# Optimization experiments

Hardware: AMD Instinct MI355X
Metric: run time of the kernel (lower is better)

The kernel has to match this reference:

```python
import jax, jax.numpy as jnp
import numpy as np

N, D, K = 16384, 256, 4096  # encoded vectors, embedding_dim, codebook_size


def setup_inputs() -> dict:
    key = jax.random.key(0)
    k_ze, k_cb = jax.random.split(key)
    ze = jax.random.normal(k_ze, (N, D), dtype=jnp.float32)
    codebook = jax.random.normal(k_cb, (K, D), dtype=jnp.float32)
    return {"ze": ze, "codebook": codebook}


def reference(ze, codebook):
    # Pairwise squared distances: ||ze||^2 + ||e||^2 - 2 ze e^T  -> [N, K]
    sq_norm = (
        jnp.sum(ze ** 2, axis=-1, keepdims=True)
        + jnp.sum(codebook ** 2, axis=1)
        - 2.0 * jnp.matmul(ze, codebook.T)
    )
    indices = jnp.argmin(sq_norm, axis=-1)            # [N]
    zq = jnp.take(codebook, indices, axis=0)          # [N, D] gather

    # VQ losses (stop-gradient mirrors .detach())
    vq_e_loss = jnp.mean((zq - jax.lax.stop_gradient(ze)) ** 2)
    vq_commit_loss = jnp.mean((jax.lax.stop_gradient(zq) - ze) ** 2)

    # perplexity: probs[i] = count_i / 10 (faithful to original, incl. /10)
    counts = jnp.zeros((K,), dtype=jnp.float32).at[indices].add(1.0)
    probs = counts / 10.0
    perplexity = jnp.exp(-jnp.sum(probs * jnp.log(probs + 1e-10)))

    return indices, zq, vq_e_loss, vq_commit_loss, perplexity
```

## Files before the change

### kernel.cpp

```cpp
#include <hip/hip_runtime.h>
#include <math.h>

#define N_TOT 16384
#define DIM   256
#define KCB   4096

typedef __attribute__((ext_vector_type(8)))  short s8v;
typedef __attribute__((ext_vector_type(16))) float f16v;

#define PK_OFF   32832
#define CBF_OFF  163904
#define WS_NEED  4358208ull
#define ZERO_W   36880

__device__ __forceinline__ void gload16(const void* g, void* l) {
  __builtin_amdgcn_global_load_lds(
      (const __attribute__((address_space(1))) unsigned int*)g,
      (__attribute__((address_space(3))) unsigned int*)l, 16, 0, 0);
}

__global__ __launch_bounds__(256)
void cb_prep_k(const float* __restrict__ cb, float* __restrict__ ws) {
  const int t = threadIdx.x, tile = blockIdx.x;
  for (int i = tile * 256 + t; i < ZERO_W; i += 128 * 256) ws[KCB + i] = 0.0f;

  const int col = t >> 3, j = t & 7;
  const int c0  = tile * 32;
  ushort* tb = (ushort*)((char*)ws + CBF_OFF) + (size_t)tile * 16384;
  const float* src = cb + (size_t)(c0 + col) * DIM;
  float s = 0.0f;
  #pragma unroll
  for (int ks = 0; ks < 16; ++ks) {
    #pragma unroll
    for (int kh = 0; kh < 2; ++kh) {
      float x = src[ks * 16 + kh * 8 + j];
      s += x * x;
      unsigned xb = __float_as_uint(x);
      unsigned hb = xb & 0xFFFF0000u;
      float lf = x - __uint_as_float(hb);
      tb[ks * 512 + kh * 256 + t]        = (ushort)(xb >> 16);
      tb[8192 + ks * 512 + kh * 256 + t] = (ushort)(__float_as_uint(lf) >> 16);
    }
  }
  s += __shfl_down(s, 4, 8);
  s += __shfl_down(s, 2, 8);
  s += __shfl_down(s, 1, 8);
  if (j == 0) ws[c0 + col] = s;
}

#define AP 260

__global__ __launch_bounds__(512, 2)
void vq_mfma_k(const float* __restrict__ ze, float* __restrict__ ws) {
  __shared__ __align__(16) char ldsU[66560];

  const int t    = threadIdx.x;
  const int lane = t & 63;
  const int w    = t >> 6;
  const int ln31 = lane & 31;
  const int hl   = lane >> 5;
  const int mb   = blockIdx.x >> 2;
  const int cq   = blockIdx.x & 3;
  const int m0   = mb * 256;

  const float* cbn = ws;
  unsigned long long* pk = (unsigned long long*)((char*)ws + PK_OFF);
  const char* cbF = (const char*)ws + CBF_OFF;

  s8v ah[16], al[16];
  float* Af = (float*)ldsU;
  for (int c = 0; c < 4; ++c) {
    __syncthreads();
    {
      int r  = t >> 3;
      int f0 = t & 7;
      const float* src = ze + (size_t)(m0 + c * 64 + r) * DIM;
      #pragma unroll
      for (int i = 0; i < 8; ++i) {
        int f = f0 + 8 * i;
        *(float4*)&Af[r * AP + f * 4] = *(const float4*)(src + f * 4);
      }
    }
    __syncthreads();
    if ((w >> 1) == c) {
      int rl = (w & 1) * 32 + ln31;
      #pragma unroll
      for (int ks = 0; ks < 16; ++ks) {
        float4 x0 = *(const float4*)&Af[rl * AP + ks * 16 + hl * 8];
        float4 x1 = *(const float4*)&Af[rl * AP + ks * 16 + hl * 8 + 4];
        float xs[8] = {x0.x, x0.y, x0.z, x0.w, x1.x, x1.y, x1.z, x1.w};
        #pragma unroll
        for (int j = 0; j < 8; ++j) {
          unsigned xb = __float_as_uint(xs[j]);
          unsigned hb = xb & 0xFFFF0000u;
          float lf = xs[j] - __uint_as_float(hb);
          ah[ks][j] = (short)(xb >> 16);
          al[ks][j] = (short)(__float_as_uint(lf) >> 16);
        }
      }
    }
  }
  __syncthreads();

  char* bufs0 = ldsU;
  char* bufs1 = ldsU + 32768;
  const char* qbase = cbF + (size_t)cq * 32 * 32768;

  {
    const char* g = qbase + (size_t)w * 4096 + (size_t)lane * 16;
    char* lp = bufs0 + w * 4096;
    #pragma unroll
    for (int ii = 0; ii < 4; ++ii) gload16(g + ii * 1024, lp + ii * 1024);
  }

  float best[16];
  int   bidx[16];
  #pragma unroll
  for (int r = 0; r < 16; ++r) { best[r] = -1e30f; bidx[r] = 0; }

  #pragma unroll 1
  for (int tt = 0; tt < 32; ++tt) {
    __syncthreads();
    if (tt + 1 < 32) {
      const char* g = qbase + (size_t)(tt + 1) * 32768 + (size_t)w * 4096 + (size_t)lane * 16;
      char* lp = ((tt + 1) & 1 ? bufs1 : bufs0) + w * 4096;
      #pragma unroll
      for (int ii = 0; ii < 4; ++ii) gload16(g + ii * 1024, lp + ii * 1024);
    }

    const int   c0      = cq * 1024 + tt * 32;
    const float half_cv = 0.5f * cbn[c0 + ln31];
    const char* bc      = (tt & 1) ? bufs1 : bufs0;

    f16v hh, xx;
    #pragma unroll
    for (int r = 0; r < 16; ++r) { hh[r] = 0.0f; xx[r] = 0.0f; }

    #pragma unroll
    for (int ks = 0; ks < 16; ++ks) {
      s8v bh = *(const s8v*)(bc + ks * 1024 + lane * 16);
      s8v bl = *(const s8v*)(bc + 16384 + ks * 1024 + lane * 16);
      hh = __builtin_amdgcn_mfma_f32_32x32x16_bf16(ah[ks], bh, hh, 0, 0, 0);
      xx = __builtin_amdgcn_mfma_f32_32x32x16_bf16(ah[ks], bl, xx, 0, 0, 0);
      xx = __builtin_amdgcn_mfma_f32_32x32x16_bf16(al[ks], bh, xx, 0, 0, 0);
    }

    #pragma unroll
    for (int r = 0; r < 16; ++r) {
      float s = hh[r] + xx[r] - half_cv;
      if (s > best[r]) { best[r] = s; bidx[r] = c0 + ln31; }
    }
  }

  #pragma unroll
  for (int r = 0; r < 16; ++r) {
    float s = best[r];
    int   c = bidx[r];
    #pragma unroll
    for (int mk = 1; mk < 32; mk <<= 1) {
      float os = __shfl_xor(s, mk, 64);
      int   oc = __shfl_xor(c, mk, 64);
      if (os > s || (os == s && oc < c)) { s = os; c = oc; }
    }
    if (ln31 == 0) {
      int row = m0 + w * 32 + (r & 3) + 8 * (r >> 2) + 4 * hl;
      unsigned u = __float_as_uint(s);
      unsigned enc = (u & 0x80000000u) ? ~u : (u | 0x80000000u);
      unsigned long long p = ((unsigned long long)enc << 32) | (unsigned)(KCB - 1 - c);
      atomicMax(&pk[row], p);
    }
  }
}

__global__ __launch_bounds__(256)
void gather_k(const float* __restrict__ ze, const float* __restrict__ cb,
              float* __restrict__ ws, float* __restrict__ out) {
  __shared__ int sIdx[64];
  const int t  = threadIdx.x;
  const int m0 = blockIdx.x * 64;
  float* counts   = ws + KCB;
  float* loss_sum = ws + 2 * KCB;
  const unsigned long long* pk = (const unsigned long long*)((const char*)ws + PK_OFF);

  if (t < 64) {
    unsigned long long p = pk[m0 + t];
    int col = KCB - 1 - (int)(unsigned)(p & 0xFFFFFFFFull);
    out[m0 + t] = (float)col;
    sIdx[t] = col;
    atomicAdd(&counts[col], 1.0f);
  }
  __syncthreads();

  float* out_zq = out + N_TOT;
  const int w = t >> 6, ln = t & 63;
  float lsum = 0.0f;
  #pragma unroll
  for (int p = 0; p < 16; ++p) {
    int r = w + 4 * p;
    float4 cvv = *(const float4*)(cb + (size_t)sIdx[r] * DIM + ln * 4);
    float4 zv  = *(const float4*)(ze + (size_t)(m0 + r) * DIM + ln * 4);
    *(float4*)(out_zq + (size_t)(m0 + r) * DIM + ln * 4) = cvv;
    float dx = cvv.x - zv.x, dy = cvv.y - zv.y, dz = cvv.z - zv.z, dw = cvv.w - zv.w;
    lsum += dx * dx + dy * dy + dz * dz + dw * dw;
  }
  #pragma unroll
  for (int off = 32; off > 0; off >>= 1) lsum += __shfl_down(lsum, off, 64);
  if (ln == 0) atomicAdd(loss_sum, lsum);
}

__global__ void zero_ws_k(float* __restrict__ ws, int nw) {
  int i = blockIdx.x * 256 + threadIdx.x;
  if (i < nw) ws[KCB + i] = 0.0f;
}

__global__ void cbnorm_k(const float* __restrict__ cb, float* __restrict__ ws) {
  int row  = blockIdx.x * 4 + (threadIdx.x >> 6);
  int lane = threadIdx.x & 63;
  float4 v = *(const float4*)(cb + (size_t)row * DIM + lane * 4);
  float s = v.x*v.x + v.y*v.y + v.z*v.z + v.w*v.w;
  #pragma unroll
  for (int off = 32; off > 0; off >>= 1) s += __shfl_down(s, off, 64);
  if (lane == 0) ws[row] = s;
}

#define FBM 32
#define FBN 64
#define FBD 128
__global__ __launch_bounds__(256, 4)
void vq_main_k(const float* __restrict__ ze, const float* __restrict__ cb,
               float* __restrict__ ws, float* __restrict__ out) {
  __shared__ float As[FBM * FBD];
  __shared__ float Bs[FBN * FBD];
  __shared__ float red_d[FBM * 16];
  __shared__ int   red_i[FBM * 16];
  __shared__ int   sIdx[FBM];

  const int t  = threadIdx.x;
  const int tx = t & 15;
  const int ty = t >> 4;
  const int m0 = blockIdx.x * FBM;

  const float* cbn = ws;
  float* counts    = ws + KCB;
  float* loss_sum  = ws + 2 * KCB;

  float best0 = 1e30f, best1 = 1e30f;
  int   bidx0 = 0,     bidx1 = 0;
  const int sA = ty & 7;
  const int sB = tx & 7;

  for (int kt = 0; kt < KCB / FBN; ++kt) {
    float cbnj[4];
    #pragma unroll
    for (int j = 0; j < 4; ++j) cbnj[j] = cbn[kt * FBN + tx + 16 * j];
    float acc[2][4];
    #pragma unroll
    for (int i = 0; i < 2; ++i)
      #pragma unroll
      for (int j = 0; j < 4; ++j) acc[i][j] = 0.0f;

    for (int dc = 0; dc < DIM / FBD; ++dc) {
      __syncthreads();
      {
        int c  = t & 31;
        int rb = t >> 5;
        #pragma unroll
        for (int p = 0; p < 4; ++p) {
          int r = rb + 8 * p;
          float4 v = *(const float4*)(ze + (size_t)(m0 + r) * DIM + dc * FBD + c * 4);
          *(float4*)&As[r * FBD + ((c ^ (r & 7)) << 2)] = v;
        }
        #pragma unroll
        for (int p = 0; p < 8; ++p) {
          int r = rb + 8 * p;
          float4 v = *(const float4*)(cb + (size_t)(kt * FBN + r) * DIM + dc * FBD + c * 4);
          *(float4*)&Bs[r * FBD + ((c ^ (r & 7)) << 2)] = v;
        }
      }
      __syncthreads();
      #pragma unroll 8
      for (int ds = 0; ds < FBD / 4; ++ds) {
        float4 a0 = *(const float4*)&As[ty * FBD + ((ds ^ sA) << 2)];
        float4 a1 = *(const float4*)&As[(ty + 16) * FBD + ((ds ^ sA) << 2)];
        float4 b[4];
        #pragma unroll
        for (int j = 0; j < 4; ++j)
          b[j] = *(const float4*)&Bs[(tx + 16 * j) * FBD + ((ds ^ sB) << 2)];
        #pragma unroll
        for (int j = 0; j < 4; ++j) {
          acc[0][j] = fmaf(a0.x, b[j].x, acc[0][j]);
          acc[0][j] = fmaf(a0.y, b[j].y, acc[0][j]);
          acc[0][j] = fmaf(a0.z, b[j].z, acc[0][j]);
          acc[0][j] = fmaf(a0.w, b[j].w, acc[0][j]);
          acc[1][j] = fmaf(a1.x, b[j].x, acc[1][j]);
          acc[1][j] = fmaf(a1.y, b[j].y, acc[1][j]);
          acc[1][j] = fmaf(a1.z, b[j].z, acc[1][j]);
          acc[1][j] = fmaf(a1.w, b[j].w, acc[1][j]);
        }
      }
    }
    #pragma unroll
    for (int j = 0; j < 4; ++j) {
      int kg = kt * FBN + tx + 16 * j;
      float d0 = cbnj[j] - 2.0f * acc[0][j];
      float d1 = cbnj[j] - 2.0f * acc[1][j];
      if (d0 < best0) { best0 = d0; bidx0 = kg; }
      if (d1 < best1) { best1 = d1; bidx1 = kg; }
    }
  }

  __syncthreads();
  red_d[ty * 16 + tx] = best0;        red_i[ty * 16 + tx] = bidx0;
  red_d[(ty + 16) * 16 + tx] = best1; red_i[(ty + 16) * 16 + tx] = bidx1;
  __syncthreads();

  if (t < FBM) {
    float bd = red_d[t * 16]; int bi = red_i[t * 16];
    #pragma unroll
    for (int q = 1; q < 16; ++q) {
      float d = red_d[t * 16 + q]; int i2 = red_i[t * 16 + q];
      if (d < bd || (d == bd && i2 < bi)) { bd = d; bi = i2; }
    }
    out[m0 + t] = (float)bi;
    sIdx[t] = bi;
    atomicAdd(&counts[bi], 1.0f);
  }
  __syncthreads();

  float* out_zq = out + N_TOT;
  const int wv = t >> 6, ln = t & 63;
  float lsum = 0.0f;
  #pragma unroll
  for (int p = 0; p < 8; ++p) {
    int r = wv + 4 * p;
    float4 cvv = *(const float4*)(cb + (size_t)sIdx[r] * DIM + ln * 4);
    float4 zv  = *(const float4*)(ze + (size_t)(m0 + r) * DIM + ln * 4);
    *(float4*)(out_zq + (size_t)(m0 + r) * DIM + ln * 4) = cvv;
    float dx = cvv.x - zv.x, dy = cvv.y - zv.y, dz = cvv.z - zv.z, dw = cvv.w - zv.w;
    lsum += dx*dx + dy*dy + dz*dz + dw*dw;
  }
  #pragma unroll
  for (int off = 32; off > 0; off >>= 1) lsum += __shfl_down(lsum, off, 64);
  if (ln == 0) atomicAdd(loss_sum, lsum);
}

__global__ void finalize_k(const float* __restrict__ ws, float* __restrict__ out) {
  __shared__ float red[256];
  int t = threadIdx.x;
  const float* counts = ws + KCB;
  float s = 0.0f;
  for (int k = t; k < KCB; k += 256) {
    float p = counts[k] * 0.1f;
    s += p * logf(p + 1e-10f);
  }
  red[t] = s;
  __syncthreads();
  for (int q = 128; q > 0; q >>= 1) { if (t < q) red[t] += red[t + q]; __syncthreads(); }
  if (t == 0) {
    float loss = ws[2 * KCB] / (float)((size_t)N_TOT * DIM);
    float* o = out + N_TOT + (size_t)N_TOT * DIM;
    o[0] = loss;
    o[1] = loss;
    o[2] = expf(-red[0]);
  }
}

extern "C" void kernel_launch(void* const* d_in, const int* in_sizes, int n_in,
                              void* d_out, int out_size, void* d_ws, size_t ws_size,
                              hipStream_t stream) {
  const float* ze = (const float*)d_in[0];
  const float* cb = (const float*)d_in[1];
  float* out = (float*)d_out;
  float* ws  = (float*)d_ws;

  if (ws_size >= WS_NEED) {
    cb_prep_k<<<128, 256, 0, stream>>>(cb, ws);
    vq_mfma_k<<<256, 512, 0, stream>>>(ze, ws);
    gather_k<<<N_TOT / 64, 256, 0, stream>>>(ze, cb, ws, out);
  } else {
    zero_ws_k<<<(KCB + 1 + 255) / 256, 256, 0, stream>>>(ws, KCB + 1);
    cbnorm_k<<<KCB / 4, 256, 0, stream>>>(cb, ws);
    vq_main_k<<<N_TOT / FBM, 256, 0, stream>>>(ze, cb, ws, out);
  }
  finalize_k<<<1, 256, 0, stream>>>(ws, out);
}
```

Baseline: 193.9 us.

## Halve VQ block size to 256 threads, stage codebook via LDS in prep

The main distance kernel now uses 256-thread blocks covering 128 rows each, with 512 blocks and the block index remapped so codebook quarter is the outer index. Codebook tile loads are redistributed across fewer waves, and the codebook norm for the next tile is prefetched into a register. cb_prep_k stages codebook rows through LDS with coalesced float4 loads, and gather_k uses smaller 32-row blocks for more parallelism. The aim is better occupancy and load balance across CUs, but each block now reuses every codebook tile for fewer rows, so global and LDS traffic per MFMA goes up.

```diff
diff --git a/kernel.cpp b/kernel.cpp
--- a/kernel.cpp
+++ b/kernel.cpp
@@ -21,19 +21,29 @@
 
 __global__ __launch_bounds__(256)
 void cb_prep_k(const float* __restrict__ cb, float* __restrict__ ws) {
+  __shared__ float Cf[32 * 260];
   const int t = threadIdx.x, tile = blockIdx.x;
   for (int i = tile * 256 + t; i < ZERO_W; i += 128 * 256) ws[KCB + i] = 0.0f;
 
+  const int c0 = tile * 32;
+  {
+    int r = t >> 3, q = t & 7;
+    const float4* src4 = (const float4*)(cb + (size_t)(c0 + r) * DIM);
+    float4* dst = (float4*)&Cf[r * 260];
+    #pragma unroll
+    for (int i = 0; i < 8; ++i) dst[q + 8 * i] = src4[q + 8 * i];
+  }
+  __syncthreads();
+
   const int col = t >> 3, j = t & 7;
-  const int c0  = tile * 32;
   ushort* tb = (ushort*)((char*)ws + CBF_OFF) + (size_t)tile * 16384;
-  const float* src = cb + (size_t)(c0 + col) * DIM;
+  const float* rowp = Cf + col * 260;
   float s = 0.0f;
   #pragma unroll
   for (int ks = 0; ks < 16; ++ks) {
     #pragma unroll
     for (int kh = 0; kh < 2; ++kh) {
-      float x = src[ks * 16 + kh * 8 + j];
+      float x = rowp[ks * 16 + kh * 8 + j];
       s += x * x;
       unsigned xb = __float_as_uint(x);
       unsigned hb = xb & 0xFFFF0000u;
@@ -48,9 +58,7 @@
   if (j == 0) ws[c0 + col] = s;
 }
 
-#define AP 260
-
-__global__ __launch_bounds__(512, 2)
+__global__ __launch_bounds__(256, 2)
 void vq_mfma_k(const float* __restrict__ ze, float* __restrict__ ws) {
   __shared__ __align__(16) char ldsU[66560];
 
@@ -59,9 +67,9 @@
   const int w    = t >> 6;
   const int ln31 = lane & 31;
   const int hl   = lane >> 5;
-  const int mb   = blockIdx.x >> 2;
-  const int cq   = blockIdx.x & 3;
-  const int m0   = mb * 256;
+  const int cq   = blockIdx.x >> 7;
+  const int mb   = blockIdx.x & 127;
+  const int m0   = mb * 128;
 
   const float* cbn = ws;
   unsigned long long* pk = (unsigned long long*)((char*)ws + PK_OFF);
@@ -69,25 +77,24 @@
 
   s8v ah[16], al[16];
   float* Af = (float*)ldsU;
-  for (int c = 0; c < 4; ++c) {
+  #pragma unroll 1
+  for (int ph = 0; ph < 2; ++ph) {
     __syncthreads();
     {
-      int r  = t >> 3;
-      int f0 = t & 7;
-      const float* src = ze + (size_t)(m0 + c * 64 + r) * DIM;
+      int r = t >> 2, q = t & 3;
+      const float4* src4 = (const float4*)(ze + (size_t)(m0 + ph * 64 + r) * DIM);
+      float4* dst = (float4*)&Af[r * 260];
       #pragma unroll
-      for (int i = 0; i < 8; ++i) {
-        int f = f0 + 8 * i;
-        *(float4*)&Af[r * AP + f * 4] = *(const float4*)(src + f * 4);
-      }
+      for (int i = 0; i < 16; ++i) dst[q + 4 * i] = src4[q + 4 * i];
     }
     __syncthreads();
-    if ((w >> 1) == c) {
+    if ((w >> 1) == ph) {
       int rl = (w & 1) * 32 + ln31;
+      const float* rowp = Af + rl * 260;
       #pragma unroll
       for (int ks = 0; ks < 16; ++ks) {
-        float4 x0 = *(const float4*)&Af[rl * AP + ks * 16 + hl * 8];
-        float4 x1 = *(const float4*)&Af[rl * AP + ks * 16 + hl * 8 + 4];
+        float4 x0 = *(const float4*)(rowp + ks * 16 + hl * 8);
+        float4 x1 = *(const float4*)(rowp + ks * 16 + hl * 8 + 4);
         float xs[8] = {x0.x, x0.y, x0.z, x0.w, x1.x, x1.y, x1.z, x1.w};
         #pragma unroll
         for (int j = 0; j < 8; ++j) {
@@ -107,11 +114,14 @@
   const char* qbase = cbF + (size_t)cq * 32 * 32768;
 
   {
-    const char* g = qbase + (size_t)w * 4096 + (size_t)lane * 16;
-    char* lp = bufs0 + w * 4096;
-    #pragma unroll
-    for (int ii = 0; ii < 4; ++ii) gload16(g + ii * 1024, lp + ii * 1024);
-  }
+    const char* g = qbase + (size_t)w * 1024 + (size_t)(lane & 63) * 16;
+    char* lp = bufs0 + w * 1024 + (lane & 63) * 0;
+    #pragma unroll
+    for (int ii = 0; ii < 8; ++ii) gload16(g + ii * 4096, bufs0 + w * 1024 + ii * 4096);
+    (void)lp;
+  }
+
+  float cvn = cbn[cq * 1024 + ln31];
 
   float best[16];
   int   bidx[16];
@@ -122,15 +132,15 @@
   for (int tt = 0; tt < 32; ++tt) {
     __syncthreads();
     if (tt + 1 < 32) {
-      const char* g = qbase + (size_t)(tt + 1) * 32768 + (size_t)w * 4096 + (size_t)lane * 16;
-      char* lp = ((tt + 1) & 1 ? bufs1 : bufs0) + w * 4096;
+      const char* g = qbase + (size_t)(tt + 1) * 32768 + (size_t)w * 1024 + (size_t)lane * 16;
+      char* lp = ((tt + 1) & 1 ? bufs1 : bufs0) + w * 1024;
       #pragma unroll
-      for (int ii = 0; ii < 4; ++ii) gload16(g + ii * 1024, lp + ii * 1024);
-    }
-
-    const int   c0      = cq * 1024 + tt * 32;
-    const float half_cv = 0.5f * cbn[c0 + ln31];
-    const char* bc      = (tt & 1) ? bufs1 : bufs0;
+      for (int ii = 0; ii < 8; ++ii) gload16(g + ii * 4096, lp + ii * 4096);
+    }
+
+    const float half_cv = 0.5f * cvn;
+    if (tt + 1 < 32) cvn = cbn[cq * 1024 + (tt + 1) * 32 + ln31];
+    const char* bc = (tt & 1) ? bufs1 : bufs0;
 
     f16v hh, xx;
     #pragma unroll
@@ -145,10 +155,11 @@
       xx = __builtin_amdgcn_mfma_f32_32x32x16_bf16(al[ks], bh, xx, 0, 0, 0);
     }
 
+    const int c0 = cq * 1024 + tt * 32 + ln31;
     #pragma unroll
     for (int r = 0; r < 16; ++r) {
       float s = hh[r] + xx[r] - half_cv;
-      if (s > best[r]) { best[r] = s; bidx[r] = c0 + ln31; }
+      if (s > best[r]) { best[r] = s; bidx[r] = c0; }
     }
   }
 
@@ -175,14 +186,14 @@
 __global__ __launch_bounds__(256)
 void gather_k(const float* __restrict__ ze, const float* __restrict__ cb,
               float* __restrict__ ws, float* __restrict__ out) {
-  __shared__ int sIdx[64];
+  __shared__ int sIdx[32];
   const int t  = threadIdx.x;
-  const int m0 = blockIdx.x * 64;
+  const int m0 = blockIdx.x * 32;
   float* counts   = ws + KCB;
   float* loss_sum = ws + 2 * KCB;
   const unsigned long long* pk = (const unsigned long long*)((const char*)ws + PK_OFF);
 
-  if (t < 64) {
+  if (t < 32) {
     unsigned long long p = pk[m0 + t];
     int col = KCB - 1 - (int)(unsigned)(p & 0xFFFFFFFFull);
     out[m0 + t] = (float)col;
@@ -195,7 +206,7 @@
   const int w = t >> 6, ln = t & 63;
   float lsum = 0.0f;
   #pragma unroll
-  for (int p = 0; p < 16; ++p) {
+  for (int p = 0; p < 8; ++p) {
     int r = w + 4 * p;
     float4 cvv = *(const float4*)(cb + (size_t)sIdx[r] * DIM + ln * 4);
     float4 zv  = *(const float4*)(ze + (size_t)(m0 + r) * DIM + ln * 4);
@@ -375,8 +386,8 @@
 
   if (ws_size >= WS_NEED) {
     cb_prep_k<<<128, 256, 0, stream>>>(cb, ws);
-    vq_mfma_k<<<256, 512, 0, stream>>>(ze, ws);
-    gather_k<<<N_TOT / 64, 256, 0, stream>>>(ze, cb, ws, out);
+    vq_mfma_k<<<512, 256, 0, stream>>>(ze, ws);
+    gather_k<<<N_TOT / 32, 256, 0, stream>>>(ze, cb, ws, out);
   } else {
     zero_ws_k<<<(KCB + 1 + 255) / 256, 256, 0, stream>>>(ws, KCB + 1);
     cbnorm_k<<<KCB / 4, 256, 0, stream>>>(cb, ws);
```

After: 208.7 us. 7.6% more time.
